# Kernel tuning notes

Hardware: AMD Instinct MI355X
Metric: run time of the kernel (lower is better)

Reference implementation:

```python
import jax, jax.numpy as jnp
import numpy as np

H = 4        # num_heads
R = 5        # dilation_rate
W = 49       # window_size
D = 256      # d_model // 2
B = 32
N = 4900     # must be divisible by W*R = 245


def setup_inputs() -> dict:
    key = jax.random.key(0)
    k1, k2, k3, k4, k5 = jax.random.split(key, 5)
    s = 1.0 / np.sqrt(D)
    return {
        "emb": jax.random.normal(k1, (B, N, D), dtype=jnp.float32),
        "Wq": jax.random.normal(k2, (D, D), dtype=jnp.float32) * s,
        "bq": jax.random.normal(k3, (D,), dtype=jnp.float32) * s,
        "Wo": jax.random.normal(k4, (D, D), dtype=jnp.float32) * s,
        "bo": jax.random.normal(k5, (D,), dtype=jnp.float32) * s,
    }


def reference(emb, Wq, bq, Wo, bo):
    b, n, d = emb.shape
    dh = d // H
    g = n // (W * R)  # number of segments
    # Original forward uses q_proj for q, k AND v (faithful to source bug).
    q = emb @ Wq.T + bq  # [B, N, D]
    # Dilated local windows: token index = g*(W*R) + i*R + r.
    # Tokens sharing (segment g, dilation offset r) attend densely over i in [0, W).
    x = q.reshape(b, g, W, R, H, dh)
    scale = jnp.asarray(dh, q.dtype) ** -0.5
    scores = jnp.einsum("bgirhd,bgjrhd->bgrhij", x, x) * scale  # [B,G,R,H,W,W]
    attn = jax.nn.softmax(scores, axis=-1)
    out = jnp.einsum("bgrhij,bgjrhd->bgirhd", attn, x)  # [B,G,W,R,H,dh]
    out = out.reshape(b, n, d)
    return out @ Wo.T + bo
```

## Files before the change

### kernel.cpp

```cpp
#include <hip/hip_runtime.h>
#include <hip/hip_bf16.h>
#include <math.h>

#define NH     4
#define RD     5
#define WW     49
#define DMODEL 256
#define BATCH  32
#define NTOK   4900
#define DH     64
#define GSEG   20
#define MROWS  (BATCH * NTOK)

typedef short bf16x8 __attribute__((ext_vector_type(8)));
typedef short bf16x4 __attribute__((ext_vector_type(4)));
typedef float f32x4  __attribute__((ext_vector_type(4)));

__device__ __forceinline__ void gl_lds16(const void* g, void* l) {
    __builtin_amdgcn_global_load_lds(
        (const __attribute__((address_space(1))) void*)g,
        (__attribute__((address_space(3))) void*)l, 16, 0, 0);
}

__device__ __forceinline__ short f2bf(float f) {
    union { __hip_bfloat16 h; short s; } u;
    u.h = __float2bfloat16(f);
    return u.s;
}

__global__ __launch_bounds__(256)
void wcvt(const float* __restrict__ Wq, const float* __restrict__ Wo,
          short* __restrict__ Wqb, short* __restrict__ Wob) {
    int t = blockIdx.x * 256 + threadIdx.x;
    const float* src = (t < 16384) ? Wq : Wo;
    short* dst = (t < 16384) ? Wqb : Wob;
    int i = (t & 16383) * 4;
    float4 v = *(const float4*)(src + i);
    bf16x4 o = { f2bf(v.x), f2bf(v.y), f2bf(v.z), f2bf(v.w) };
    *(bf16x4*)(dst + i) = o;
}

__global__ __launch_bounds__(256)
void gemm1_mfma(const float* __restrict__ A, const short* __restrict__ Bw,
                const float* __restrict__ bias, __hip_bfloat16* __restrict__ C) {
    __shared__ __align__(16) short As[128 * 32];
    __shared__ __align__(16) short Bs[128 * 32];
    const int tid = threadIdx.x;
    const int wv = tid >> 6, ln = tid & 63;
    const int lc = ln & 15, lq = ln >> 4;
    const int m0 = blockIdx.y * 128, n0 = blockIdx.x * 128;
    const int wm = (wv & 1) * 64, wn = (wv >> 1) * 64;

    f32x4 acc[4][4] = {};

    const int arow = tid >> 3, akc = (tid & 7) * 4;

    for (int k0 = 0; k0 < DMODEL; k0 += 32) {
        #pragma unroll
        for (int rr = 0; rr < 4; rr++) {
            const int row = rr * 32 + arow;
            float4 v = *(const float4*)(A + (size_t)(m0 + row) * DMODEL + k0 + akc);
            bf16x4 o = { f2bf(v.x), f2bf(v.y), f2bf(v.z), f2bf(v.w) };
            *(bf16x4*)&As[row * 32 + akc] = o;
        }
        #pragma unroll
        for (int cc = 0; cc < 2; cc++) {
            const int c = wv + cc * 4;
            gl_lds16(Bw + (size_t)(n0 + c * 16 + (ln >> 2)) * DMODEL + k0 + (ln & 3) * 8,
                     &Bs[c * 512]);
        }
        __syncthreads();

        bf16x8 af[4], bf[4];
        #pragma unroll
        for (int mi = 0; mi < 4; mi++)
            af[mi] = *(const bf16x8*)&As[(wm + mi * 16 + lc) * 32 + lq * 8];
        #pragma unroll
        for (int ni = 0; ni < 4; ni++)
            bf[ni] = *(const bf16x8*)&Bs[(wn + ni * 16 + lc) * 32 + lq * 8];
        #pragma unroll
        for (int mi = 0; mi < 4; mi++)
            #pragma unroll
            for (int ni = 0; ni < 4; ni++)
                acc[mi][ni] = __builtin_amdgcn_mfma_f32_16x16x32_bf16(
                    af[mi], bf[ni], acc[mi][ni], 0, 0, 0);
        __syncthreads();
    }

    float bv[4];
    #pragma unroll
    for (int ni = 0; ni < 4; ni++) bv[ni] = bias[n0 + wn + ni * 16 + lc];
    #pragma unroll
    for (int mi = 0; mi < 4; mi++)
        #pragma unroll
        for (int rg = 0; rg < 4; rg++) {
            const int row = m0 + wm + mi * 16 + lq * 4 + rg;
            #pragma unroll
            for (int ni = 0; ni < 4; ni++)
                C[(size_t)row * DMODEL + n0 + wn + ni * 16 + lc] =
                    __float2bfloat16(acc[mi][ni][rg] + bv[ni]);
        }
}

__global__ __launch_bounds__(256)
void gemm2_mfma(const short* __restrict__ A, const short* __restrict__ Bw,
                const float* __restrict__ bias, float* __restrict__ C) {
    __shared__ __align__(16) short As[128 * 32];
    __shared__ __align__(16) short Bs[128 * 32];
    const int tid = threadIdx.x;
    const int wv = tid >> 6, ln = tid & 63;
    const int lc = ln & 15, lq = ln >> 4;
    const int m0 = blockIdx.y * 128, n0 = blockIdx.x * 128;
    const int wm = (wv & 1) * 64, wn = (wv >> 1) * 64;

    f32x4 acc[4][4] = {};

    for (int k0 = 0; k0 < DMODEL; k0 += 32) {
        #pragma unroll
        for (int cc = 0; cc < 2; cc++) {
            const int c = wv + cc * 4;
            gl_lds16(A + (size_t)(m0 + c * 16 + (ln >> 2)) * DMODEL + k0 + (ln & 3) * 8,
                     &As[c * 512]);
            gl_lds16(Bw + (size_t)(n0 + c * 16 + (ln >> 2)) * DMODEL + k0 + (ln & 3) * 8,
                     &Bs[c * 512]);
        }
        __syncthreads();

        bf16x8 af[4], bf[4];
        #pragma unroll
        for (int mi = 0; mi < 4; mi++)
            af[mi] = *(const bf16x8*)&As[(wm + mi * 16 + lc) * 32 + lq * 8];
        #pragma unroll
        for (int ni = 0; ni < 4; ni++)
            bf[ni] = *(const bf16x8*)&Bs[(wn + ni * 16 + lc) * 32 + lq * 8];
        #pragma unroll
        for (int mi = 0; mi < 4; mi++)
            #pragma unroll
            for (int ni = 0; ni < 4; ni++)
                acc[mi][ni] = __builtin_amdgcn_mfma_f32_16x16x32_bf16(
                    af[mi], bf[ni], acc[mi][ni], 0, 0, 0);
        __syncthreads();
    }

    float bv[4];
    #pragma unroll
    for (int ni = 0; ni < 4; ni++) bv[ni] = bias[n0 + wn + ni * 16 + lc];
    #pragma unroll
    for (int mi = 0; mi < 4; mi++)
        #pragma unroll
        for (int rg = 0; rg < 4; rg++) {
            const int row = m0 + wm + mi * 16 + lq * 4 + rg;
            #pragma unroll
            for (int ni = 0; ni < 4; ni++)
                C[(size_t)row * DMODEL + n0 + wn + ni * 16 + lc] =
                    acc[mi][ni][rg] + bv[ni];
        }
}

__global__ __launch_bounds__(256)
void attn_mfma(short* __restrict__ q) {
    const int bid = blockIdx.x;
    const int h = bid & 3;
    const int r = (bid >> 2) % RD;
    const int g = (bid / (NH * RD)) % GSEG;
    const int b = bid / (NH * RD * GSEG);

    __shared__ __align__(16) short X [64 * 72];
    __shared__ __align__(16) short XT[64 * 72];
    __shared__ __align__(16) short SP[64 * 72];

    const int tid = threadIdx.x;
    const int wv = tid >> 6, ln = tid & 63;
    const int lc = ln & 15, lq = ln >> 4;
    const size_t base = ((size_t)(b * NTOK + g * (WW * RD) + r)) * DMODEL + h * DH;

    for (int p = tid; p < 15 * 64; p += 256)
        X[(49 + (p >> 6)) * 72 + (p & 63)] = 0;
    for (int p = tid; p < 64 * 15; p += 256)
        XT[(p / 15) * 72 + 49 + (p % 15)] = 0;

    #pragma unroll
    for (int pass = 0; pass < 2; pass++) {
        const int i = pass * 32 + (tid >> 3), ch = tid & 7;
        if (i < WW) {
            bf16x8 v = *(const bf16x8*)(q + base + (size_t)i * (RD * DMODEL) + ch * 8);
            *(bf16x8*)&X[i * 72 + ch * 8] = v;
            #pragma unroll
            for (int j = 0; j < 8; j++) XT[(ch * 8 + j) * 72 + i] = v[j];
        }
    }
    __syncthreads();

    f32x4 sa[4] = {};
    {
        const bf16x8 a0 = *(const bf16x8*)&X[(16 * wv + lc) * 72 + lq * 8];
        const bf16x8 a1 = *(const bf16x8*)&X[(16 * wv + lc) * 72 + 32 + lq * 8];
        #pragma unroll
        for (int ni = 0; ni < 4; ni++) {
            const bf16x8 b0 = *(const bf16x8*)&X[(ni * 16 + lc) * 72 + lq * 8];
            const bf16x8 b1 = *(const bf16x8*)&X[(ni * 16 + lc) * 72 + 32 + lq * 8];
            sa[ni] = __builtin_amdgcn_mfma_f32_16x16x32_bf16(a0, b0, sa[ni], 0, 0, 0);
            sa[ni] = __builtin_amdgcn_mfma_f32_16x16x32_bf16(a1, b1, sa[ni], 0, 0, 0);
        }
    }

    #pragma unroll
    for (int rg = 0; rg < 4; rg++) {
        float s[4];
        float m = -1e30f;
        #pragma unroll
        for (int ni = 0; ni < 4; ni++) {
            s[ni] = sa[ni][rg] * 0.125f;
            if (ni * 16 + lc < WW) m = fmaxf(m, s[ni]);
        }
        m = fmaxf(m, __shfl_xor(m, 1));
        m = fmaxf(m, __shfl_xor(m, 2));
        m = fmaxf(m, __shfl_xor(m, 4));
        m = fmaxf(m, __shfl_xor(m, 8));
        float e[4], l_ = 0.f;
        #pragma unroll
        for (int ni = 0; ni < 4; ni++) {
            e[ni] = (ni * 16 + lc < WW) ? __expf(s[ni] - m) : 0.f;
            l_ += e[ni];
        }
        l_ += __shfl_xor(l_, 1);
        l_ += __shfl_xor(l_, 2);
        l_ += __shfl_xor(l_, 4);
        l_ += __shfl_xor(l_, 8);
        const float inv = 1.f / l_;
        const int row = 16 * wv + lq * 4 + rg;
        #pragma unroll
        for (int ni = 0; ni < 4; ni++)
            SP[row * 72 + ni * 16 + lc] = f2bf(e[ni] * inv);
    }

    f32x4 oa[4] = {};
    {
        const bf16x8 a0 = *(const bf16x8*)&SP[(16 * wv + lc) * 72 + lq * 8];
        const bf16x8 a1 = *(const bf16x8*)&SP[(16 * wv + lc) * 72 + 32 + lq * 8];
        #pragma unroll
        for (int ni = 0; ni < 4; ni++) {
            const bf16x8 b0 = *(const bf16x8*)&XT[(ni * 16 + lc) * 72 + lq * 8];
            const bf16x8 b1 = *(const bf16x8*)&XT[(ni * 16 + lc) * 72 + 32 + lq * 8];
            oa[ni] = __builtin_amdgcn_mfma_f32_16x16x32_bf16(a0, b0, oa[ni], 0, 0, 0);
            oa[ni] = __builtin_amdgcn_mfma_f32_16x16x32_bf16(a1, b1, oa[ni], 0, 0, 0);
        }
    }

    __hip_bfloat16* qb = (__hip_bfloat16*)q;
    #pragma unroll
    for (int rg = 0; rg < 4; rg++) {
        const int i = 16 * wv + lq * 4 + rg;
        if (i < WW) {
            #pragma unroll
            for (int ni = 0; ni < 4; ni++)
                qb[base + (size_t)i * (RD * DMODEL) + ni * 16 + lc] =
                    __float2bfloat16(oa[ni][rg]);
        }
    }
}

extern "C" void kernel_launch(void* const* d_in, const int* in_sizes, int n_in,
                              void* d_out, int out_size, void* d_ws, size_t ws_size,
                              hipStream_t stream) {
    const float* emb = (const float*)d_in[0];
    const float* Wq  = (const float*)d_in[1];
    const float* bq  = (const float*)d_in[2];
    const float* Wo  = (const float*)d_in[3];
    const float* bo  = (const float*)d_in[4];
    float* out = (float*)d_out;

    short* q = (short*)d_ws;
    const size_t q_elems = (size_t)MROWS * DMODEL;
    short* Wqb = q + q_elems;
    short* Wob = Wqb + DMODEL * DMODEL;

    wcvt<<<dim3(128), dim3(256), 0, stream>>>(Wq, Wo, Wqb, Wob);

    dim3 gg(DMODEL / 128, MROWS / 128);
    gemm1_mfma<<<gg, dim3(256), 0, stream>>>(emb, Wqb, bq, (__hip_bfloat16*)q);
    attn_mfma<<<dim3(BATCH * GSEG * RD * NH), dim3(256), 0, stream>>>(q);
    gemm2_mfma<<<gg, dim3(256), 0, stream>>>(q, Wob, bo, out);
}
```

Before: 395.1 us.

## Fuse Q projection, dilated window attention and output projection into one segment kernel

Replaces the three-kernel pipeline (GEMM1, attention, GEMM2) with one kernel per (batch, segment). Each kernel keeps the 245x256 bf16 Q tile in XOR-swizzled shared memory, runs all 20 (r,h) attention windows in place, then does the output projection straight from shared memory. This removes the global round-trips of the bf16 intermediate and two launches. In exchange it uses about 154KB of LDS per block, which limits occupancy. The GEMM operands are also loaded directly from global memory into registers without LDS staging, and the row tile is padded from 245 to 256 rows.

```diff
diff --git a/kernel.cpp b/kernel.cpp
--- a/kernel.cpp
+++ b/kernel.cpp
@@ -5,27 +5,30 @@
 #define NH     4
 #define RD     5
 #define WW     49
-#define DMODEL 256
+#define DM     256
 #define BATCH  32
 #define NTOK   4900
-#define DH     64
 #define GSEG   20
-#define MROWS  (BATCH * NTOK)
+#define SEG    245
 
 typedef short bf16x8 __attribute__((ext_vector_type(8)));
 typedef short bf16x4 __attribute__((ext_vector_type(4)));
 typedef float f32x4  __attribute__((ext_vector_type(4)));
-
-__device__ __forceinline__ void gl_lds16(const void* g, void* l) {
-    __builtin_amdgcn_global_load_lds(
-        (const __attribute__((address_space(1))) void*)g,
-        (__attribute__((address_space(3))) void*)l, 16, 0, 0);
-}
 
 __device__ __forceinline__ short f2bf(float f) {
     union { __hip_bfloat16 h; short s; } u;
     u.h = __float2bfloat16(f);
     return u.s;
+}
+
+__device__ __forceinline__ int qix(int row, int col) {
+    return row * 256 + (col ^ ((row & 7) << 3));
+}
+__device__ __forceinline__ int xix(int d, int j) {
+    return d * 64 + (j ^ ((((d >> 3) ^ d) & 7) << 3));
+}
+__device__ __forceinline__ int pix(int i, int j) {
+    return i * 64 + (j ^ ((i & 7) << 3));
 }
 
 __global__ __launch_bounds__(256)
@@ -40,223 +43,202 @@
     *(bf16x4*)(dst + i) = o;
 }
 
-__global__ __launch_bounds__(256)
-void gemm1_mfma(const float* __restrict__ A, const short* __restrict__ Bw,
-                const float* __restrict__ bias, __hip_bfloat16* __restrict__ C) {
-    __shared__ __align__(16) short As[128 * 32];
-    __shared__ __align__(16) short Bs[128 * 32];
+__global__ __launch_bounds__(512, 2)
+void fused(const float* __restrict__ emb, const short* __restrict__ Wqb,
+           const float* __restrict__ bq, const short* __restrict__ Wob,
+           const float* __restrict__ bo, float* __restrict__ out) {
+    __shared__ __align__(16) short smem[SEG * DM + 4 * 4096];
+    short* q_s = smem;
+
     const int tid = threadIdx.x;
-    const int wv = tid >> 6, ln = tid & 63;
-    const int lc = ln & 15, lq = ln >> 4;
-    const int m0 = blockIdx.y * 128, n0 = blockIdx.x * 128;
-    const int wm = (wv & 1) * 64, wn = (wv >> 1) * 64;
-
-    f32x4 acc[4][4] = {};
-
-    const int arow = tid >> 3, akc = (tid & 7) * 4;
-
-    for (int k0 = 0; k0 < DMODEL; k0 += 32) {
-        #pragma unroll
-        for (int rr = 0; rr < 4; rr++) {
-            const int row = rr * 32 + arow;
-            float4 v = *(const float4*)(A + (size_t)(m0 + row) * DMODEL + k0 + akc);
-            bf16x4 o = { f2bf(v.x), f2bf(v.y), f2bf(v.z), f2bf(v.w) };
-            *(bf16x4*)&As[row * 32 + akc] = o;
-        }
-        #pragma unroll
-        for (int cc = 0; cc < 2; cc++) {
-            const int c = wv + cc * 4;
-            gl_lds16(Bw + (size_t)(n0 + c * 16 + (ln >> 2)) * DMODEL + k0 + (ln & 3) * 8,
-                     &Bs[c * 512]);
-        }
-        __syncthreads();
-
-        bf16x8 af[4], bf[4];
+    const int wv = tid >> 6, ln = tid & 63, lc = ln & 15, lq = ln >> 4;
+    const int b = blockIdx.x / GSEG, g = blockIdx.x % GSEG;
+    const size_t ebase = ((size_t)b * NTOK + (size_t)g * SEG) * DM;
+
+    const int wm = (wv & 3) * 64;
+    const int wn = (wv >> 2) * 128;
+
+    {
+        const float* ar[4];
+        const short* br[8];
+        #pragma unroll
+        for (int mi = 0; mi < 4; mi++) {
+            int t = wm + mi * 16 + lc;
+            t = (t > SEG - 1) ? (SEG - 1) : t;
+            ar[mi] = emb + ebase + (size_t)t * DM + lq * 8;
+        }
+        #pragma unroll
+        for (int ni = 0; ni < 8; ni++)
+            br[ni] = Wqb + (size_t)(wn + ni * 16 + lc) * DM + lq * 8;
+
+        f32x4 acc[4][8] = {};
+        for (int k0 = 0; k0 < DM; k0 += 32) {
+            bf16x8 af[4], bfr[8];
+            #pragma unroll
+            for (int mi = 0; mi < 4; mi++) {
+                float4 v0 = *(const float4*)(ar[mi] + k0);
+                float4 v1 = *(const float4*)(ar[mi] + k0 + 4);
+                bf16x8 t8 = { f2bf(v0.x), f2bf(v0.y), f2bf(v0.z), f2bf(v0.w),
+                              f2bf(v1.x), f2bf(v1.y), f2bf(v1.z), f2bf(v1.w) };
+                af[mi] = t8;
+            }
+            #pragma unroll
+            for (int ni = 0; ni < 8; ni++) bfr[ni] = *(const bf16x8*)(br[ni] + k0);
+            #pragma unroll
+            for (int mi = 0; mi < 4; mi++)
+                #pragma unroll
+                for (int ni = 0; ni < 8; ni++)
+                    acc[mi][ni] = __builtin_amdgcn_mfma_f32_16x16x32_bf16(
+                        af[mi], bfr[ni], acc[mi][ni], 0, 0, 0);
+        }
+        float bv[8];
+        #pragma unroll
+        for (int ni = 0; ni < 8; ni++) bv[ni] = bq[wn + ni * 16 + lc];
         #pragma unroll
         for (int mi = 0; mi < 4; mi++)
-            af[mi] = *(const bf16x8*)&As[(wm + mi * 16 + lc) * 32 + lq * 8];
-        #pragma unroll
-        for (int ni = 0; ni < 4; ni++)
-            bf[ni] = *(const bf16x8*)&Bs[(wn + ni * 16 + lc) * 32 + lq * 8];
-        #pragma unroll
-        for (int mi = 0; mi < 4; mi++)
-            #pragma unroll
-            for (int ni = 0; ni < 4; ni++)
-                acc[mi][ni] = __builtin_amdgcn_mfma_f32_16x16x32_bf16(
-                    af[mi], bf[ni], acc[mi][ni], 0, 0, 0);
-        __syncthreads();
-    }
-
-    float bv[4];
-    #pragma unroll
-    for (int ni = 0; ni < 4; ni++) bv[ni] = bias[n0 + wn + ni * 16 + lc];
-    #pragma unroll
-    for (int mi = 0; mi < 4; mi++)
-        #pragma unroll
-        for (int rg = 0; rg < 4; rg++) {
-            const int row = m0 + wm + mi * 16 + lq * 4 + rg;
-            #pragma unroll
-            for (int ni = 0; ni < 4; ni++)
-                C[(size_t)row * DMODEL + n0 + wn + ni * 16 + lc] =
-                    __float2bfloat16(acc[mi][ni][rg] + bv[ni]);
-        }
-}
-
-__global__ __launch_bounds__(256)
-void gemm2_mfma(const short* __restrict__ A, const short* __restrict__ Bw,
-                const float* __restrict__ bias, float* __restrict__ C) {
-    __shared__ __align__(16) short As[128 * 32];
-    __shared__ __align__(16) short Bs[128 * 32];
-    const int tid = threadIdx.x;
-    const int wv = tid >> 6, ln = tid & 63;
-    const int lc = ln & 15, lq = ln >> 4;
-    const int m0 = blockIdx.y * 128, n0 = blockIdx.x * 128;
-    const int wm = (wv & 1) * 64, wn = (wv >> 1) * 64;
-
-    f32x4 acc[4][4] = {};
-
-    for (int k0 = 0; k0 < DMODEL; k0 += 32) {
-        #pragma unroll
-        for (int cc = 0; cc < 2; cc++) {
-            const int c = wv + cc * 4;
-            gl_lds16(A + (size_t)(m0 + c * 16 + (ln >> 2)) * DMODEL + k0 + (ln & 3) * 8,
-                     &As[c * 512]);
-            gl_lds16(Bw + (size_t)(n0 + c * 16 + (ln >> 2)) * DMODEL + k0 + (ln & 3) * 8,
-                     &Bs[c * 512]);
-        }
-        __syncthreads();
-
-        bf16x8 af[4], bf[4];
-        #pragma unroll
-        for (int mi = 0; mi < 4; mi++)
-            af[mi] = *(const bf16x8*)&As[(wm + mi * 16 + lc) * 32 + lq * 8];
-        #pragma unroll
-        for (int ni = 0; ni < 4; ni++)
-            bf[ni] = *(const bf16x8*)&Bs[(wn + ni * 16 + lc) * 32 + lq * 8];
-        #pragma unroll
-        for (int mi = 0; mi < 4; mi++)
-            #pragma unroll
-            for (int ni = 0; ni < 4; ni++)
-                acc[mi][ni] = __builtin_amdgcn_mfma_f32_16x16x32_bf16(
-                    af[mi], bf[ni], acc[mi][ni], 0, 0, 0);
-        __syncthreads();
-    }
-
-    float bv[4];
-    #pragma unroll
-    for (int ni = 0; ni < 4; ni++) bv[ni] = bias[n0 + wn + ni * 16 + lc];
-    #pragma unroll
-    for (int mi = 0; mi < 4; mi++)
-        #pragma unroll
-        for (int rg = 0; rg < 4; rg++) {
-            const int row = m0 + wm + mi * 16 + lq * 4 + rg;
-            #pragma unroll
-            for (int ni = 0; ni < 4; ni++)
-                C[(size_t)row * DMODEL + n0 + wn + ni * 16 + lc] =
-                    acc[mi][ni][rg] + bv[ni];
-        }
-}
-
-__global__ __launch_bounds__(256)
-void attn_mfma(short* __restrict__ q) {
-    const int bid = blockIdx.x;
-    const int h = bid & 3;
-    const int r = (bid >> 2) % RD;
-    const int g = (bid / (NH * RD)) % GSEG;
-    const int b = bid / (NH * RD * GSEG);
-
-    __shared__ __align__(16) short X [64 * 72];
-    __shared__ __align__(16) short XT[64 * 72];
-    __shared__ __align__(16) short SP[64 * 72];
-
-    const int tid = threadIdx.x;
-    const int wv = tid >> 6, ln = tid & 63;
-    const int lc = ln & 15, lq = ln >> 4;
-    const size_t base = ((size_t)(b * NTOK + g * (WW * RD) + r)) * DMODEL + h * DH;
-
-    for (int p = tid; p < 15 * 64; p += 256)
-        X[(49 + (p >> 6)) * 72 + (p & 63)] = 0;
-    for (int p = tid; p < 64 * 15; p += 256)
-        XT[(p / 15) * 72 + 49 + (p % 15)] = 0;
-
-    #pragma unroll
-    for (int pass = 0; pass < 2; pass++) {
-        const int i = pass * 32 + (tid >> 3), ch = tid & 7;
-        if (i < WW) {
-            bf16x8 v = *(const bf16x8*)(q + base + (size_t)i * (RD * DMODEL) + ch * 8);
-            *(bf16x8*)&X[i * 72 + ch * 8] = v;
-            #pragma unroll
-            for (int j = 0; j < 8; j++) XT[(ch * 8 + j) * 72 + i] = v[j];
-        }
+            #pragma unroll
+            for (int rg = 0; rg < 4; rg++) {
+                const int t = wm + mi * 16 + lq * 4 + rg;
+                if (t < SEG) {
+                    const int lr = (t % RD) * WW + t / RD;
+                    #pragma unroll
+                    for (int ni = 0; ni < 8; ni++)
+                        q_s[qix(lr, wn + ni * 16 + lc)] =
+                            f2bf(acc[mi][ni][rg] + bv[ni]);
+                }
+            }
     }
     __syncthreads();
 
-    f32x4 sa[4] = {};
     {
-        const bf16x8 a0 = *(const bf16x8*)&X[(16 * wv + lc) * 72 + lq * 8];
-        const bf16x8 a1 = *(const bf16x8*)&X[(16 * wv + lc) * 72 + 32 + lq * 8];
-        #pragma unroll
-        for (int ni = 0; ni < 4; ni++) {
-            const bf16x8 b0 = *(const bf16x8*)&X[(ni * 16 + lc) * 72 + lq * 8];
-            const bf16x8 b1 = *(const bf16x8*)&X[(ni * 16 + lc) * 72 + 32 + lq * 8];
-            sa[ni] = __builtin_amdgcn_mfma_f32_16x16x32_bf16(a0, b0, sa[ni], 0, 0, 0);
-            sa[ni] = __builtin_amdgcn_mfma_f32_16x16x32_bf16(a1, b1, sa[ni], 0, 0, 0);
+        const int tm = wv >> 2, tv = wv & 3, ttid = tid & 255;
+        short* xt = smem + SEG * DM + tm * 4096;
+        short* sp = smem + SEG * DM + 8192 + tm * 4096;
+        for (int rr = 0; rr < 10; rr++) {
+            const int gi = rr * 2 + tm, r = gi >> 2, c0 = (gi & 3) * 64;
+
+            #pragma unroll
+            for (int u0 = 0; u0 < 2; u0++) {
+                const int u = ttid + u0 * 256, j = u >> 3, dc = (u & 7) * 8;
+                bf16x8 v = (bf16x8){0, 0, 0, 0, 0, 0, 0, 0};
+                if (j < WW) v = *(const bf16x8*)&q_s[qix(r * WW + j, c0 + dc)];
+                #pragma unroll
+                for (int e = 0; e < 8; e++) xt[xix(dc + e, j)] = v[e];
+            }
+            f32x4 sa[4] = {};
+            {
+                const int arw = r * WW + tv * 16 + lc;
+                const bf16x8 a0 = *(const bf16x8*)&q_s[qix(arw, c0 + lq * 8)];
+                const bf16x8 a1 = *(const bf16x8*)&q_s[qix(arw, c0 + 32 + lq * 8)];
+                #pragma unroll
+                for (int ni = 0; ni < 4; ni++) {
+                    const int brw = r * WW + ni * 16 + lc;
+                    const bf16x8 b0 = *(const bf16x8*)&q_s[qix(brw, c0 + lq * 8)];
+                    const bf16x8 b1 = *(const bf16x8*)&q_s[qix(brw, c0 + 32 + lq * 8)];
+                    sa[ni] = __builtin_amdgcn_mfma_f32_16x16x32_bf16(a0, b0, sa[ni], 0, 0, 0);
+                    sa[ni] = __builtin_amdgcn_mfma_f32_16x16x32_bf16(a1, b1, sa[ni], 0, 0, 0);
+                }
+            }
+            __syncthreads();
+
+            #pragma unroll
+            for (int rg = 0; rg < 4; rg++) {
+                float s[4];
+                float m = -1e30f;
+                #pragma unroll
+                for (int ni = 0; ni < 4; ni++) {
+                    s[ni] = sa[ni][rg] * 0.125f;
+                    if (ni * 16 + lc < WW) m = fmaxf(m, s[ni]);
+                }
+                m = fmaxf(m, __shfl_xor(m, 1));
+                m = fmaxf(m, __shfl_xor(m, 2));
+                m = fmaxf(m, __shfl_xor(m, 4));
+                m = fmaxf(m, __shfl_xor(m, 8));
+                float e4[4], l_ = 0.f;
+                #pragma unroll
+                for (int ni = 0; ni < 4; ni++) {
+                    e4[ni] = (ni * 16 + lc < WW) ? __expf(s[ni] - m) : 0.f;
+                    l_ += e4[ni];
+                }
+                l_ += __shfl_xor(l_, 1);
+                l_ += __shfl_xor(l_, 2);
+                l_ += __shfl_xor(l_, 4);
+                l_ += __shfl_xor(l_, 8);
+                const float inv = 1.f / l_;
+                const int pr = tv * 16 + lq * 4 + rg;
+                #pragma unroll
+                for (int ni = 0; ni < 4; ni++)
+                    sp[pix(pr, ni * 16 + lc)] = f2bf(e4[ni] * inv);
+            }
+            f32x4 oa[4] = {};
+            {
+                const int arw = tv * 16 + lc;
+                const bf16x8 a0 = *(const bf16x8*)&sp[pix(arw, lq * 8)];
+                const bf16x8 a1 = *(const bf16x8*)&sp[pix(arw, 32 + lq * 8)];
+                #pragma unroll
+                for (int ni = 0; ni < 4; ni++) {
+                    const int d = ni * 16 + lc;
+                    const bf16x8 b0 = *(const bf16x8*)&xt[xix(d, lq * 8)];
+                    const bf16x8 b1 = *(const bf16x8*)&xt[xix(d, 32 + lq * 8)];
+                    oa[ni] = __builtin_amdgcn_mfma_f32_16x16x32_bf16(a0, b0, oa[ni], 0, 0, 0);
+                    oa[ni] = __builtin_amdgcn_mfma_f32_16x16x32_bf16(a1, b1, oa[ni], 0, 0, 0);
+                }
+            }
+            #pragma unroll
+            for (int rg = 0; rg < 4; rg++) {
+                const int i = tv * 16 + lq * 4 + rg;
+                if (i < WW) {
+                    #pragma unroll
+                    for (int ni = 0; ni < 4; ni++)
+                        q_s[qix(r * WW + i, c0 + ni * 16 + lc)] = f2bf(oa[ni][rg]);
+                }
+            }
+            __syncthreads();
         }
     }
 
-    #pragma unroll
-    for (int rg = 0; rg < 4; rg++) {
-        float s[4];
-        float m = -1e30f;
-        #pragma unroll
-        for (int ni = 0; ni < 4; ni++) {
-            s[ni] = sa[ni][rg] * 0.125f;
-            if (ni * 16 + lc < WW) m = fmaxf(m, s[ni]);
-        }
-        m = fmaxf(m, __shfl_xor(m, 1));
-        m = fmaxf(m, __shfl_xor(m, 2));
-        m = fmaxf(m, __shfl_xor(m, 4));
-        m = fmaxf(m, __shfl_xor(m, 8));
-        float e[4], l_ = 0.f;
-        #pragma unroll
-        for (int ni = 0; ni < 4; ni++) {
-            e[ni] = (ni * 16 + lc < WW) ? __expf(s[ni] - m) : 0.f;
-            l_ += e[ni];
-        }
-        l_ += __shfl_xor(l_, 1);
-        l_ += __shfl_xor(l_, 2);
-        l_ += __shfl_xor(l_, 4);
-        l_ += __shfl_xor(l_, 8);
-        const float inv = 1.f / l_;
-        const int row = 16 * wv + lq * 4 + rg;
-        #pragma unroll
-        for (int ni = 0; ni < 4; ni++)
-            SP[row * 72 + ni * 16 + lc] = f2bf(e[ni] * inv);
-    }
-
-    f32x4 oa[4] = {};
     {
-        const bf16x8 a0 = *(const bf16x8*)&SP[(16 * wv + lc) * 72 + lq * 8];
-        const bf16x8 a1 = *(const bf16x8*)&SP[(16 * wv + lc) * 72 + 32 + lq * 8];
-        #pragma unroll
-        for (int ni = 0; ni < 4; ni++) {
-            const bf16x8 b0 = *(const bf16x8*)&XT[(ni * 16 + lc) * 72 + lq * 8];
-            const bf16x8 b1 = *(const bf16x8*)&XT[(ni * 16 + lc) * 72 + 32 + lq * 8];
-            oa[ni] = __builtin_amdgcn_mfma_f32_16x16x32_bf16(a0, b0, oa[ni], 0, 0, 0);
-            oa[ni] = __builtin_amdgcn_mfma_f32_16x16x32_bf16(a1, b1, oa[ni], 0, 0, 0);
-        }
-    }
-
-    __hip_bfloat16* qb = (__hip_bfloat16*)q;
-    #pragma unroll
-    for (int rg = 0; rg < 4; rg++) {
-        const int i = 16 * wv + lq * 4 + rg;
-        if (i < WW) {
-            #pragma unroll
-            for (int ni = 0; ni < 4; ni++)
-                qb[base + (size_t)i * (RD * DMODEL) + ni * 16 + lc] =
-                    __float2bfloat16(oa[ni][rg]);
-        }
+        const short* br[8];
+        #pragma unroll
+        for (int ni = 0; ni < 8; ni++)
+            br[ni] = Wob + (size_t)(wn + ni * 16 + lc) * DM + lq * 8;
+        int lr[4];
+        #pragma unroll
+        for (int mi = 0; mi < 4; mi++) {
+            int t = wm + mi * 16 + lc;
+            t = (t > SEG - 1) ? (SEG - 1) : t;
+            lr[mi] = (t % RD) * WW + t / RD;
+        }
+        f32x4 acc[4][8] = {};
+        for (int k0 = 0; k0 < DM; k0 += 32) {
+            bf16x8 af[4], bfr[8];
+            #pragma unroll
+            for (int mi = 0; mi < 4; mi++)
+                af[mi] = *(const bf16x8*)&q_s[qix(lr[mi], k0 + lq * 8)];
+            #pragma unroll
+            for (int ni = 0; ni < 8; ni++) bfr[ni] = *(const bf16x8*)(br[ni] + k0);
+            #pragma unroll
+            for (int mi = 0; mi < 4; mi++)
+                #pragma unroll
+                for (int ni = 0; ni < 8; ni++)
+                    acc[mi][ni] = __builtin_amdgcn_mfma_f32_16x16x32_bf16(
+                        af[mi], bfr[ni], acc[mi][ni], 0, 0, 0);
+        }
+        float bv[8];
+        #pragma unroll
+        for (int ni = 0; ni < 8; ni++) bv[ni] = bo[wn + ni * 16 + lc];
+        #pragma unroll
+        for (int mi = 0; mi < 4; mi++)
+            #pragma unroll
+            for (int rg = 0; rg < 4; rg++) {
+                const int t = wm + mi * 16 + lq * 4 + rg;
+                if (t < SEG) {
+                    float* op = out + ebase + (size_t)t * DM;
+                    #pragma unroll
+                    for (int ni = 0; ni < 8; ni++)
+                        op[wn + ni * 16 + lc] = acc[mi][ni][rg] + bv[ni];
+                }
+            }
     }
 }
 
@@ -270,15 +252,9 @@
     const float* bo  = (const float*)d_in[4];
     float* out = (float*)d_out;
 
-    short* q = (short*)d_ws;
-    const size_t q_elems = (size_t)MROWS * DMODEL;
-    short* Wqb = q + q_elems;
-    short* Wob = Wqb + DMODEL * DMODEL;
+    short* Wqb = (short*)d_ws;
+    short* Wob = Wqb + DM * DM;
 
     wcvt<<<dim3(128), dim3(256), 0, stream>>>(Wq, Wo, Wqb, Wob);
-
-    dim3 gg(DMODEL / 128, MROWS / 128);
-    gemm1_mfma<<<gg, dim3(256), 0, stream>>>(emb, Wqb, bq, (__hip_bfloat16*)q);
-    attn_mfma<<<dim3(BATCH * GSEG * RD * NH), dim3(256), 0, stream>>>(q);
-    gemm2_mfma<<<gg, dim3(256), 0, stream>>>(q, Wob, bo, out);
-}
+    fused<<<dim3(BATCH * GSEG), dim3(512), 0, stream>>>(emb, Wqb, bq, Wob, bo, out);
+}
```

Result: slower. 467.2 us (+18.2%).
